# Performance work log

Hardware: AMD Instinct MI355X
Metric: run time of the kernel (lower is better)

Reference implementation:

```python
import jax, jax.numpy as jnp
import numpy as np

B, M, L = 100, 100, 8
N = M * L
EPS = 1e-5  # torch BatchNorm2d default eps


def _conv(x, w, b, stride, pad):
    y = jax.lax.conv_general_dilated(x, w, (stride, stride), [(pad, pad), (pad, pad)],
                                     dimension_numbers=('NCHW', 'OIHW', 'NCHW'))
    return y + b[None, :, None, None]


def _convT(x, w, b, stride, pad):
    # torch ConvTranspose2d weight layout: (in_ch, out_ch, kH, kW)
    k = w.shape[2]
    wt = jnp.flip(w, (2, 3)).transpose(1, 0, 2, 3)  # -> OIHW
    p = k - 1 - pad
    y = jax.lax.conv_general_dilated(x, wt, (1, 1), [(p, p), (p, p)],
                                     lhs_dilation=(stride, stride),
                                     dimension_numbers=('NCHW', 'OIHW', 'NCHW'))
    return y + b[None, :, None, None]


def _bn(x):
    # BatchNorm2d constructed fresh in forward: weight=1, bias=0, batch stats (biased var)
    mean = x.mean(axis=(0, 2, 3), keepdims=True)
    var = x.var(axis=(0, 2, 3), keepdims=True)
    return (x - mean) / jnp.sqrt(var + EPS)


def _leaky(x):
    return jnp.where(x >= 0, x, 0.01 * x)


def _forward(x, conv1_w, conv1_b, conv2_w, conv2_b, conv3_w, conv3_b, conv4_w, conv4_b,
             fc_w, fc_b, dec_w, dec_b, ct1_w, ct1_b, ct2_w, ct2_b, ct3_w, ct3_b,
             ct4_w, ct4_b, ct5_w, ct5_b):
    # ---- encoder ----
    h = _bn(_leaky(_conv(x, conv1_w, conv1_b, 2, 1)))   # (B,128,32,32)
    h = _bn(_leaky(_conv(h, conv2_w, conv2_b, 2, 1)))   # (B,256,16,16)
    h = _bn(_leaky(_conv(h, conv3_w, conv3_b, 2, 1)))   # (B,1024,8,8)
    h = _bn(_leaky(_conv(h, conv4_w, conv4_b, 2, 1)))   # (B,1024,4,4)
    eig = jax.nn.relu(h.reshape(B, -1) @ fc_w + fc_b)   # (B, 800)
    # ---- latent_sample (training branch) ----
    sig = eig.reshape(B, M, L)
    row = jnp.sqrt(float(M * L)) * jnp.fft.ifft2(sig)          # complex (B,M,L)
    # original builds C via numpy/scipy per-sample -> detached; circulant[i,j] = c[(i-j) % n]
    row_flat = jax.lax.stop_gradient(row.real.reshape(B, N))
    i = jnp.arange(N)
    idx = (i[:, None] - i[None, :]) % N                        # (N,N) circulant gather
    C = row_flat[:, idx]                                       # (B,N,N)
    # original: Sigma_batch_eps[:, i] = eigenvalue (noise zeta is dead code), via numpy -> detached
    Y = jnp.fft.fft2(jax.lax.stop_gradient(sig)).real          # (B,M,L)
    # ---- decoder ----
    d = (Y.reshape(B, N) @ dec_w + dec_b).reshape(B, 1024, 3, 3)
    d = _convT(d, ct1_w, ct1_b, 2, 1)   # (B,512,5,5)
    d = _convT(d, ct2_w, ct2_b, 2, 0)   # (B,256,11,11)
    d = _convT(d, ct3_w, ct3_b, 2, 0)   # (B,128,23,23)
    d = _convT(d, ct4_w, ct4_b, 2, 0)   # (B,64,47,47)
    d = _convT(d, ct5_w, ct5_b, 1, 0)   # (B,1,49,49)
    return d, C, eig


def setup_inputs():
    key = jax.random.key(0)
    ks = jax.random.split(key, 16)

    def wv(k, shape, fan_in):
        return (jax.random.normal(k, shape, jnp.float32) / np.sqrt(fan_in)).astype(jnp.float32)

    return {
        'x': jax.random.normal(ks[0], (B, 1, 64, 64), jnp.float32),
        'conv1_w': wv(ks[1], (128, 1, 3, 3), 9), 'conv1_b': jnp.zeros((128,), jnp.float32),
        'conv2_w': wv(ks[2], (256, 128, 3, 3), 128 * 9), 'conv2_b': jnp.zeros((256,), jnp.float32),
        'conv3_w': wv(ks[3], (1024, 256, 3, 3), 256 * 9), 'conv3_b': jnp.zeros((1024,), jnp.float32),
        'conv4_w': wv(ks[4], (1024, 1024, 3, 3), 1024 * 9), 'conv4_b': jnp.zeros((1024,), jnp.float32),
        'fc_w': wv(ks[5], (1024 * 16, N), 1024 * 16), 'fc_b': jnp.zeros((N,), jnp.float32),
        'dec_w': wv(ks[6], (N, 1024 * 9), N), 'dec_b': jnp.zeros((1024 * 9,), jnp.float32),
        'ct1_w': wv(ks[7], (1024, 512, 3, 3), 1024 * 9), 'ct1_b': jnp.zeros((512,), jnp.float32),
        'ct2_w': wv(ks[8], (512, 256, 3, 3), 512 * 9), 'ct2_b': jnp.zeros((256,), jnp.float32),
        'ct3_w': wv(ks[9], (256, 128, 3, 3), 256 * 9), 'ct3_b': jnp.zeros((128,), jnp.float32),
        'ct4_w': wv(ks[10], (128, 64, 3, 3), 128 * 9), 'ct4_b': jnp.zeros((64,), jnp.float32),
        'ct5_w': wv(ks[11], (64, 1, 3, 3), 64 * 9), 'ct5_b': jnp.zeros((1,), jnp.float32),
    }


def reference(x, conv1_w, conv1_b, conv2_w, conv2_b, conv3_w, conv3_b, conv4_w, conv4_b,
              fc_w, fc_b, dec_w, dec_b, ct1_w, ct1_b, ct2_w, ct2_b, ct3_w, ct3_b,
              ct4_w, ct4_b, ct5_w, ct5_b):
    return _forward(x, conv1_w, conv1_b, conv2_w, conv2_b, conv3_w, conv3_b, conv4_w, conv4_b,
                    fc_w, fc_b, dec_w, dec_b, ct1_w, ct1_b, ct2_w, ct2_b, ct3_w, ct3_b,
                    ct4_w, ct4_b, ct5_w, ct5_b)
```

## Files before the change

### kernel.cpp

```cpp
#include <hip/hip_runtime.h>
#include <math.h>

typedef __attribute__((ext_vector_type(8))) short bf16x8;
typedef __attribute__((ext_vector_type(4))) float f32x4;
typedef unsigned short u16;

__device__ __forceinline__ u16 f2bf(float f) {
    unsigned u = __builtin_bit_cast(unsigned, f);
    u += 0x7FFFu + ((u >> 16) & 1u);
    return (u16)(u >> 16);
}
__device__ __forceinline__ float bf2f(u16 h) {
    unsigned u = ((unsigned)h) << 16;
    return __builtin_bit_cast(float, u);
}

template<int MODE, int OUT, int BM, int BN, int SWIZ, bool STATS, bool PF>
__global__ __launch_bounds__(256, 3)
void gemm(const u16* __restrict__ Abf, const u16* __restrict__ Bw,
          const float* __restrict__ bias, void* __restrict__ outv,
          float* __restrict__ stat,
          int M, int N, int K, int lgC,
          int IH, int IW, int OH, int OW, int zchunk)
{
    constexpr int ANSEG = BM / 64, BNSEG = BN / 64;
    constexpr int RM = BM / 32, RN = BN / 32;
    __shared__ __align__(16) u16 As[4 * BM * 8];
    __shared__ __align__(16) u16 Bs[4 * BN * 8];
    const int t = threadIdx.x;
    const int lane = t & 63, wave = t >> 6;
    const int lm = lane & 15, quad = lane >> 4;
    const int wm = wave & 1, wn = wave >> 1;
    int mt, nt, z;
    if (SWIZ == 1) {
        int mtN = (M + BM - 1) / BM;
        int id = blockIdx.x;
        nt = id & 7; int j = id >> 3;
        mt = j % mtN; z = j / mtN;
    } else { mt = blockIdx.x; nt = blockIdx.y; z = blockIdx.z; }
    const int k0 = z * zchunk, kend = k0 + zchunk;

    const int arow = (ANSEG == 2) ? (t >> 1) : (t >> 2);
    const int akb  = (ANSEG == 2) ? (t & 1) * 16 : (t & 3) * 8;
    const int a_gm = mt * BM + arow;
    const bool a_in = a_gm < M;
    int oy = 0, ox = 0, bimg = 0;
    if (MODE == 1) {
        int ohw = OH * OW;
        int g = a_in ? a_gm : 0;
        bimg = g / ohw; int r = g - bimg * ohw;
        oy = r / OW; ox = r - (r / OW) * OW;
    }
    const int brow = (BNSEG == 2) ? (t >> 1) : (t >> 2);
    const int bkb  = (BNSEG == 2) ? (t & 1) * 16 : (t & 3) * 8;
    const int b_gn = nt * BN + brow;
    const bool b_in = b_gn < N;

    const int Cmask = (1 << lgC) - 1;
    int ic_s = 0, tap_s = 0;
    bool aok = a_in;
    const u16* aptr;
    if (MODE == 0) {
        aptr = Abf + (size_t)a_gm * K + k0 + akb;
    } else {
        int kk0 = k0 + akb;
        tap_s = kk0 >> lgC; ic_s = kk0 & Cmask;
        int ky = tap_s / 3, kx = tap_s - (tap_s / 3) * 3;
        int iy = oy * 2 - 1 + ky, ix = ox * 2 - 1 + kx;
        aok = a_in && (unsigned)iy < (unsigned)IH && (unsigned)ix < (unsigned)IW;
        aptr = Abf + ((((size_t)bimg * IH + iy) * IW + ix) << lgC);
    }
    const u16* bptr = Bw + (size_t)b_gn * K + k0 + bkb;

    auto ldA = [&](uint4 (&v)[ANSEG]) {
        #pragma unroll
        for (int s = 0; s < ANSEG; s++) {
            uint4 x4 = make_uint4(0, 0, 0, 0);
            if (MODE == 0) {
                if (aok) x4 = *(const uint4*)(aptr + s * 8);
            } else {
                if (aok) x4 = *(const uint4*)(aptr + ic_s + s * 8);
            }
            v[s] = x4;
        }
        if (MODE == 0) {
            aptr += 32;
        } else {
            ic_s += 32;
            if (ic_s > Cmask) {
                ic_s -= Cmask + 1;
                tap_s++;
                int ky = tap_s / 3, kx = tap_s - (tap_s / 3) * 3;
                int iy = oy * 2 - 1 + ky, ix = ox * 2 - 1 + kx;
                aok = a_in && (unsigned)iy < (unsigned)IH && (unsigned)ix < (unsigned)IW;
                aptr = Abf + ((((size_t)bimg * IH + iy) * IW + ix) << lgC);
            }
        }
    };
    auto ldB = [&](uint4 (&v)[BNSEG]) {
        #pragma unroll
        for (int s = 0; s < BNSEG; s++) {
            uint4 x4 = make_uint4(0, 0, 0, 0);
            if (b_in) x4 = *(const uint4*)(bptr + s * 8);
            v[s] = x4;
        }
        bptr += 32;
    };

    f32x4 acc[RM][RN];
    #pragma unroll
    for (int i = 0; i < RM; i++)
        #pragma unroll
        for (int j = 0; j < RN; j++) acc[i][j] = (f32x4){0.f, 0.f, 0.f, 0.f};

    uint4 va[ANSEG], vb[BNSEG];
    if (PF) { ldA(va); ldB(vb); }
    for (int kb = k0; kb < kend; kb += 32) {
        if (!PF) { ldA(va); ldB(vb); }
        #pragma unroll
        for (int s = 0; s < ANSEG; s++)
            *(uint4*)&As[(((akb >> 3) + s) * BM + arow) * 8] = va[s];
        #pragma unroll
        for (int s = 0; s < BNSEG; s++)
            *(uint4*)&Bs[(((bkb >> 3) + s) * BN + brow) * 8] = vb[s];
        __syncthreads();
        if (PF && kb + 32 < kend) { ldA(va); ldB(vb); }
        bf16x8 af[RM], bfr[RN];
        #pragma unroll
        for (int i = 0; i < RM; i++)
            af[i] = *(const bf16x8*)&As[(size_t)(quad * BM + wm * (BM / 2) + i * 16 + lm) * 8];
        #pragma unroll
        for (int j = 0; j < RN; j++)
            bfr[j] = *(const bf16x8*)&Bs[(size_t)(quad * BN + wn * (BN / 2) + j * 16 + lm) * 8];
        #pragma unroll
        for (int i = 0; i < RM; i++)
            #pragma unroll
            for (int j = 0; j < RN; j++)
                acc[i][j] = __builtin_amdgcn_mfma_f32_16x16x32_bf16(af[i], bfr[j], acc[i][j], 0, 0, 0);
        __syncthreads();
    }

    const int n_base = nt * BN + wn * (BN / 2);
    const int m_base = mt * BM + wm * (BM / 2);
    int nj[RN]; float bvj[RN];
    #pragma unroll
    for (int j = 0; j < RN; j++) {
        nj[j] = n_base + j * 16 + lm;
        bvj[j] = 0.f;
        if (nj[j] < N && OUT != 4) {
            if (OUT == 0 || OUT == 5) bvj[j] = bias[nj[j]];
            else if (z == 0) bvj[j] = bias[nj[j]];
        }
    }
    if constexpr (OUT == 4) {
        float* op = (float*)outv;
        #pragma unroll
        for (int i = 0; i < RM; i++)
            #pragma unroll
            for (int r = 0; r < 4; r++) {
                int m = m_base + i * 16 + quad * 4 + r;
                if (m >= M) continue;
                #pragma unroll
                for (int j = 0; j < RN; j++)
                    if (nj[j] < N) atomicAdd(&op[(size_t)m * N + nj[j]], acc[i][j][r]);
            }
    } else if constexpr (OUT == 5) {
        u16* op = (u16*)outv;
        #pragma unroll
        for (int j = 0; j < RN; j++) {
            if (nj[j] >= N) continue;
            int c = nj[j] / 9, hw = nj[j] - c * 9;
            #pragma unroll
            for (int i = 0; i < RM; i++)
                #pragma unroll
                for (int r = 0; r < 4; r++) {
                    int m = m_base + i * 16 + quad * 4 + r;
                    if (m >= M) continue;
                    op[((size_t)m * 9 + hw) * 1024 + c] = f2bf(acc[i][j][r] + bvj[j]);
                }
        }
    } else if constexpr (OUT == 0) {
        int ohw = OH * OW;
        float sj[RN], qj[RN];
        #pragma unroll
        for (int j = 0; j < RN; j++) { sj[j] = 0.f; qj[j] = 0.f; }
        #pragma unroll
        for (int i = 0; i < RM; i++) {
            int m0 = m_base + i * 16 + quad * 4;
            if (m0 >= M) continue;
            int b = m0 / ohw, pix = m0 - b * ohw;
            #pragma unroll
            for (int j = 0; j < RN; j++) {
                if (nj[j] >= N) continue;
                #pragma unroll
                for (int r = 0; r < 4; r++) {
                    float val = acc[i][j][r] + bvj[j];
                    ((u16*)outv)[((size_t)b * ohw + pix + r) * N + nj[j]] = f2bf(val);
                    if (STATS) {
                        float lv = val >= 0.f ? val : 0.01f * val;
                        sj[j] += lv; qj[j] += lv * lv;
                    }
                }
            }
        }
        if constexpr (STATS) {
            #pragma unroll
            for (int j = 0; j < RN; j++) {
                float s = sj[j], q = qj[j];
                s += __shfl_down(s, 32); q += __shfl_down(q, 32);
                s += __shfl_down(s, 16); q += __shfl_down(q, 16);
                if (quad == 0 && nj[j] < N) {
                    atomicAdd(&stat[nj[j]], s);
                    atomicAdd(&stat[N + nj[j]], q);
                }
            }
        }
    } else {
        int ohw = OH * OW;
        #pragma unroll
        for (int i = 0; i < RM; i++) {
            int m0 = m_base + i * 16 + quad * 4;
            if (m0 >= M) continue;
            int b = m0 / ohw, pix = m0 - b * ohw;
            #pragma unroll
            for (int j = 0; j < RN; j++) {
                if (nj[j] >= N) continue;
                #pragma unroll
                for (int r = 0; r < 4; r++)
                    atomicAdd(&((float*)outv)[((size_t)b * ohw + pix + r) * N + nj[j]],
                              acc[i][j][r] + bvj[j]);
            }
        }
    }
}

template<int BM>
__global__ __launch_bounds__(256, 3)
void gemm_ct(const u16* __restrict__ Abf, const u16* __restrict__ Wb,
             const float* __restrict__ bias, u16* __restrict__ out,
             int N, int lgC, int IH, int IW, int OH, int OW,
             int4 Kc, int4 Mc, int4 Hc, int4 Wc, int4 Oc, int4 Dy, int4 Dx)
{
    constexpr int ANSEG = BM / 64;
    constexpr int RM = BM / 32, RN = 2;
    const int c = blockIdx.z;
    const int Ks[4] = {Kc.x, Kc.y, Kc.z, Kc.w};
    const int Ms[4] = {Mc.x, Mc.y, Mc.z, Mc.w};
    const int Hs[4] = {Hc.x, Hc.y, Hc.z, Hc.w};
    const int Wsz[4]= {Wc.x, Wc.y, Wc.z, Wc.w};
    const int Os[4] = {Oc.x, Oc.y, Oc.z, Oc.w};
    const int Dys[4]= {Dy.x, Dy.y, Dy.z, Dy.w};
    const int Dxs[4]= {Dx.x, Dx.y, Dx.z, Dx.w};
    const int K = Ks[c], M = Ms[c], OHc = Hs[c], OWc = Wsz[c];
    const int dyp = Dys[c], dxp = Dxs[c];
    const int mt = blockIdx.x, nt = blockIdx.y;
    if (mt * BM >= M) return;
    const u16* Bw = Wb + Os[c];

    __shared__ __align__(16) u16 As[4 * BM * 8];
    __shared__ __align__(16) u16 Bs[4 * 64 * 8];
    const int t = threadIdx.x;
    const int lane = t & 63, wave = t >> 6;
    const int lm = lane & 15, quad = lane >> 4;
    const int wm = wave & 1, wn = wave >> 1;

    const int arow = (ANSEG == 2) ? (t >> 1) : (t >> 2);
    const int akb  = (ANSEG == 2) ? (t & 1) * 16 : (t & 3) * 8;
    const int a_gm = mt * BM + arow;
    const bool a_in = a_gm < M;
    const int ohwc = OHc * OWc;
    int g = a_in ? a_gm : 0;
    int bimg = g / ohwc; int rr = g - bimg * ohwc;
    int oy = rr / OWc, ox = rr - (rr / OWc) * OWc;

    const int brow = t >> 2;
    const int bkb  = (t & 3) * 8;
    const int b_gn = nt * 64 + brow;
    const bool b_in = b_gn < N;

    const int Cmask = (1 << lgC) - 1;
    int ic_s = akb & Cmask;
    int ti_s = 0;
    bool aok; const u16* aptr;
    {
        int sh = 8 * (ti_s & 3);
        int dy = (int)(signed char)((dyp >> sh) & 255);
        int dx = (int)(signed char)((dxp >> sh) & 255);
        int iy = oy + dy, ix = ox + dx;
        aok = a_in && (unsigned)iy < (unsigned)IH && (unsigned)ix < (unsigned)IW;
        aptr = Abf + ((((size_t)bimg * IH + iy) * IW + ix) << lgC);
    }
    const u16* bptr = Bw + (size_t)b_gn * K + bkb;

    auto ldA = [&](uint4 (&v)[ANSEG]) {
        #pragma unroll
        for (int s = 0; s < ANSEG; s++) {
            uint4 x4 = make_uint4(0, 0, 0, 0);
            if (aok) x4 = *(const uint4*)(aptr + ic_s + s * 8);
            v[s] = x4;
        }
        ic_s += 32;
        if (ic_s > Cmask) {
            ic_s -= Cmask + 1;
            ti_s++;
            int sh = 8 * (ti_s & 3);
            int dy = (int)(signed char)((dyp >> sh) & 255);
            int dx = (int)(signed char)((dxp >> sh) & 255);
            int iy = oy + dy, ix = ox + dx;
            aok = a_in && (unsigned)iy < (unsigned)IH && (unsigned)ix < (unsigned)IW;
            aptr = Abf + ((((size_t)bimg * IH + iy) * IW + ix) << lgC);
        }
    };
    auto ldB = [&](uint4& v) {
        uint4 x4 = make_uint4(0, 0, 0, 0);
        if (b_in) x4 = *(const uint4*)bptr;
        v = x4;
        bptr += 32;
    };

    f32x4 acc[RM][RN];
    #pragma unroll
    for (int i = 0; i < RM; i++)
        #pragma unroll
        for (int j = 0; j < RN; j++) acc[i][j] = (f32x4){0.f, 0.f, 0.f, 0.f};

    uint4 va[ANSEG]; uint4 vb;
    ldA(va); ldB(vb);
    for (int kb = 0; kb < K; kb += 32) {
        #pragma unroll
        for (int s = 0; s < ANSEG; s++)
            *(uint4*)&As[(((akb >> 3) + s) * BM + arow) * 8] = va[s];
        *(uint4*)&Bs[((bkb >> 3) * 64 + brow) * 8] = vb;
        __syncthreads();
        if (kb + 32 < K) { ldA(va); ldB(vb); }
        bf16x8 af[RM], bfr[RN];
        #pragma unroll
        for (int i = 0; i < RM; i++)
            af[i] = *(const bf16x8*)&As[(size_t)(quad * BM + wm * (BM / 2) + i * 16 + lm) * 8];
        #pragma unroll
        for (int j = 0; j < RN; j++)
            bfr[j] = *(const bf16x8*)&Bs[(size_t)(quad * 64 + wn * 32 + j * 16 + lm) * 8];
        #pragma unroll
        for (int i = 0; i < RM; i++)
            #pragma unroll
            for (int j = 0; j < RN; j++)
                acc[i][j] = __builtin_amdgcn_mfma_f32_16x16x32_bf16(af[i], bfr[j], acc[i][j], 0, 0, 0);
        __syncthreads();
    }

    const int n_base = nt * 64 + wn * 32;
    const int m_base = mt * BM + wm * (BM / 2);
    const int cy = c >> 1, cx = c & 1;
    const int OHW = OH * OW;
    int nj[RN]; float bvj[RN];
    #pragma unroll
    for (int j = 0; j < RN; j++) {
        nj[j] = n_base + j * 16 + lm;
        bvj[j] = (nj[j] < N) ? bias[nj[j]] : 0.f;
    }
    #pragma unroll
    for (int i = 0; i < RM; i++)
        #pragma unroll
        for (int r = 0; r < 4; r++) {
            int m = m_base + i * 16 + quad * 4 + r;
            if (m >= M) continue;
            int b = m / ohwc, r2 = m - b * ohwc;
            int oyc = r2 / OWc, oxc = r2 - (r2 / OWc) * OWc;
            size_t ad0 = ((size_t)b * OHW + (2 * oyc + cy) * OW + 2 * oxc + cx) * N;
            #pragma unroll
            for (int j = 0; j < RN; j++)
                if (nj[j] < N) out[ad0 + nj[j]] = f2bf(acc[i][j][r] + bvj[j]);
        }
}

__global__ __launch_bounds__(256)
void convw_prep(const float* __restrict__ src, u16* __restrict__ dst, int lgC, int total) {
    int idx = blockIdx.x * 256 + threadIdx.x;
    if (idx >= total) return;
    int K = 9 << lgC;
    int oc = idx / K, kk = idx - oc * K;
    int tap = kk >> lgC, ic = kk & ((1 << lgC) - 1);
    dst[idx] = f2bf(src[(((size_t)oc << lgC) + ic) * 9 + tap]);
}

__global__ __launch_bounds__(256)
void transpose_cvt(const float* __restrict__ in, u16* __restrict__ out, int R, int C) {
    __shared__ float tl[32][33];
    int c0 = blockIdx.x * 32, r0 = blockIdx.y * 32;
    int tx = threadIdx.x & 31, ty = threadIdx.x >> 5;
    #pragma unroll
    for (int l = 0; l < 4; l++)
        tl[ty + 8 * l][tx] = in[(size_t)(r0 + ty + 8 * l) * C + c0 + tx];
    __syncthreads();
    #pragma unroll
    for (int l = 0; l < 4; l++)
        out[(size_t)(c0 + ty + 8 * l) * R + r0 + tx] = f2bf(tl[tx][ty + 8 * l]);
}

__global__ __launch_bounds__(256)
void ctw_fused(const float* __restrict__ in, u16* __restrict__ outw,
               int CIN, int P, int4 Kc, int4 Oc) {
    __shared__ float tl[32][33];
    int c0 = blockIdx.x * 32, r0 = blockIdx.y * 32;
    int C = gridDim.x * 32;
    int tx = threadIdx.x & 31, ty = threadIdx.x >> 5;
    #pragma unroll
    for (int l = 0; l < 4; l++)
        tl[ty + 8 * l][tx] = in[(size_t)(r0 + ty + 8 * l) * C + c0 + tx];
    __syncthreads();
    const int Ks[4] = {Kc.x, Kc.y, Kc.z, Kc.w};
    const int Os[4] = {Oc.x, Oc.y, Oc.z, Oc.w};
    int ic = r0 + tx;
    #pragma unroll
    for (int l = 0; l < 4; l++) {
        int cc = c0 + ty + 8 * l;
        int oc = cc / 9, tap = cc - 9 * oc;
        int ky = tap / 3, kx = tap - 3 * (tap / 3);
        int cyc = (P + ky) & 1, cxc = (P + kx) & 1;
        int cls = cyc * 2 + cxc;
        int nkx = ((P ^ cxc) & 1) ? 1 : 2;
        int ti = (ky >> 1) * nkx + (kx >> 1);
        outw[Os[cls] + (size_t)oc * Ks[cls] + ti * CIN + ic] = f2bf(tl[tx][ty + 8 * l]);
    }
}

__global__ __launch_bounds__(256)
void fcw_prep(const float* __restrict__ in, u16* __restrict__ out) {
    __shared__ float tl[32][33];
    int n0 = blockIdx.x * 32, c0 = blockIdx.y * 32, hw = blockIdx.z;
    int tx = threadIdx.x & 31, ty = threadIdx.x >> 5;
    #pragma unroll
    for (int l = 0; l < 4; l++)
        tl[ty + 8 * l][tx] = in[((size_t)(c0 + ty + 8 * l) * 16 + hw) * 800 + n0 + tx];
    __syncthreads();
    #pragma unroll
    for (int l = 0; l < 4; l++)
        out[(size_t)(n0 + ty + 8 * l) * 16384 + hw * 1024 + c0 + tx] = f2bf(tl[tx][ty + 8 * l]);
}

__global__ __launch_bounds__(256)
void wt5_prep(const float* __restrict__ in, u16* __restrict__ out) {
    int idx = blockIdx.x * 256 + threadIdx.x;
    if (idx >= 576) return;
    int tap = idx >> 6, ic = idx & 63;
    out[idx] = f2bf(in[ic * 9 + tap]);
}

__global__ __launch_bounds__(256)
void conv1_nhwc(const float* __restrict__ x, const float* __restrict__ w,
                const float* __restrict__ bias, u16* __restrict__ out) {
    int idx = blockIdx.x * 256 + threadIdx.x;
    if (idx >= 100 * 1024 * 128) return;
    int oc = idx & 127;
    int pix = (idx >> 7) & 1023;
    int b = idx >> 17;
    int oy = pix >> 5, ox = pix & 31;
    int iy0 = oy * 2 - 1, ix0 = ox * 2 - 1;
    float acc = bias[oc];
    const float* ip = x + (size_t)b * 4096;
    const float* wp = w + oc * 9;
    #pragma unroll
    for (int ky = 0; ky < 3; ky++) {
        int iy = iy0 + ky;
        if ((unsigned)iy >= 64u) continue;
        #pragma unroll
        for (int kx = 0; kx < 3; kx++) {
            int ix = ix0 + kx;
            if ((unsigned)ix >= 64u) continue;
            acc = fmaf(ip[iy * 64 + ix], wp[ky * 3 + kx], acc);
        }
    }
    out[idx] = f2bf(acc);
}

__global__ __launch_bounds__(256)
void bnstat8(const u16* __restrict__ x, float* __restrict__ accum, int C, int total) {
    __shared__ float ls[2048];
    for (int i = threadIdx.x; i < 2 * C; i += 256) ls[i] = 0.f;
    __syncthreads();
    int base = (blockIdx.x * 256 + threadIdx.x) * 8;
    int stride = gridDim.x * 256 * 8;
    float s[8], q[8];
    #pragma unroll
    for (int r = 0; r < 8; r++) { s[r] = 0.f; q[r] = 0.f; }
    for (int i = base; i < total; i += stride) {
        uint4 v = *(const uint4*)(x + i);
        const unsigned* w = (const unsigned*)&v;
        #pragma unroll
        for (int h = 0; h < 4; h++) {
            float v0 = __builtin_bit_cast(float, w[h] << 16);
            float v1 = __builtin_bit_cast(float, w[h] & 0xFFFF0000u);
            v0 = v0 >= 0.f ? v0 : 0.01f * v0;
            v1 = v1 >= 0.f ? v1 : 0.01f * v1;
            s[2 * h] += v0;     q[2 * h] += v0 * v0;
            s[2 * h + 1] += v1; q[2 * h + 1] += v1 * v1;
        }
    }
    int c0 = base & (C - 1);
    #pragma unroll
    for (int r = 0; r < 8; r++) {
        atomicAdd(&ls[c0 + r], s[r]);
        atomicAdd(&ls[C + c0 + r], q[r]);
    }
    __syncthreads();
    for (int i = threadIdx.x; i < 2 * C; i += 256) atomicAdd(&accum[i], ls[i]);
}

__global__ __launch_bounds__(256)
void bnapply8(const u16* __restrict__ x, u16* __restrict__ out,
              const float* __restrict__ accum, int C, int total, float invcnt) {
    int i8 = (blockIdx.x * 256 + threadIdx.x) * 8;
    if (i8 >= total) return;
    int c0 = i8 & (C - 1);
    uint4 v = *(const uint4*)(x + i8);
    const unsigned* w = (const unsigned*)&v;
    uint4 o;
    unsigned* ow = (unsigned*)&o;
    #pragma unroll
    for (int h = 0; h < 4; h++) {
        float m0 = accum[c0 + 2 * h] * invcnt, m1 = accum[c0 + 2 * h + 1] * invcnt;
        float q0 = accum[C + c0 + 2 * h] * invcnt, q1 = accum[C + c0 + 2 * h + 1] * invcnt;
        float in0 = rsqrtf(q0 - m0 * m0 + 1e-5f);
        float in1 = rsqrtf(q1 - m1 * m1 + 1e-5f);
        float v0 = __builtin_bit_cast(float, w[h] << 16);
        float v1 = __builtin_bit_cast(float, w[h] & 0xFFFF0000u);
        v0 = v0 >= 0.f ? v0 : 0.01f * v0;
        v1 = v1 >= 0.f ? v1 : 0.01f * v1;
        unsigned r0 = f2bf((v0 - m0) * in0);
        unsigned r1 = f2bf((v1 - m1) * in1);
        ow[h] = r0 | (r1 << 16);
    }
    *(uint4*)(out + i8) = o;
}

__global__ __launch_bounds__(256)
void bnstat4f(const float* __restrict__ x, float* __restrict__ accum, int C, int total) {
    __shared__ float ls[2048];
    for (int i = threadIdx.x; i < 2 * C; i += 256) ls[i] = 0.f;
    __syncthreads();
    int base = (blockIdx.x * 256 + threadIdx.x) * 4;
    int stride = gridDim.x * 1024;
    float s[4] = {0, 0, 0, 0}, q[4] = {0, 0, 0, 0};
    for (int i = base; i < total; i += stride) {
        f32x4 v = *(const f32x4*)(x + i);
        #pragma unroll
        for (int r = 0; r < 4; r++) {
            float vv = v[r]; vv = vv >= 0.f ? vv : 0.01f * vv;
            s[r] += vv; q[r] += vv * vv;
        }
    }
    int c0 = base & (C - 1);
    #pragma unroll
    for (int r = 0; r < 4; r++) {
        atomicAdd(&ls[c0 + r], s[r]);
        atomicAdd(&ls[C + c0 + r], q[r]);
    }
    __syncthreads();
    for (int i = threadIdx.x; i < 2 * C; i += 256) atomicAdd(&accum[i], ls[i]);
}

__global__ __launch_bounds__(256)
void bnapply4f(const float* __restrict__ x, u16* __restrict__ out,
               const float* __restrict__ accum, int C, int total, float invcnt) {
    int i4 = (blockIdx.x * 256 + threadIdx.x) * 4;
    if (i4 >= total) return;
    int c0 = i4 & (C - 1);
    f32x4 v = *(const f32x4*)(x + i4);
    unsigned r4[4];
    #pragma unroll
    for (int r = 0; r < 4; r++) {
        float m = accum[c0 + r] * invcnt;
        float var = accum[C + c0 + r] * invcnt - m * m;
        float inv = rsqrtf(var + 1e-5f);
        float vv = v[r]; vv = vv >= 0.f ? vv : 0.01f * vv;
        r4[r] = f2bf((vv - m) * inv);
    }
    *(uint2*)(out + i4) = make_uint2(r4[0] | (r4[1] << 16), r4[2] | (r4[3] << 16));
}

__global__ __launch_bounds__(256)
void finalize_relu(const float* __restrict__ acc, const float* __restrict__ bias,
                   float* __restrict__ out) {
    int i = blockIdx.x * 256 + threadIdx.x;
    if (i >= 100 * 800) return;
    float v = acc[i] + bias[i % 800];
    out[i] = fmaxf(v, 0.f);
}

__global__ __launch_bounds__(256)
void dft_real(const float* __restrict__ eig, float* __restrict__ Yr, u16* __restrict__ Yrb) {
    __shared__ float se[800];
    __shared__ float ctab[800];
    int b = blockIdx.x;
    for (int i = threadIdx.x; i < 800; i += 256) {
        se[i] = eig[b * 800 + i];
        ctab[i] = cospif(i * 0.0025f);
    }
    __syncthreads();
    int o0 = blockIdx.y * 400;
    for (int oi = o0 + threadIdx.x; oi < o0 + 400; oi += 256) {
        int k1 = oi >> 3, k2 = oi & 7;
        int d1 = k1 * 8, d2 = k2 * 100;
        float acc0 = 0.f, acc1 = 0.f;
        int p1 = 0;
        for (int n1 = 0; n1 < 100; n1 += 2) {
            int p = p1;
            #pragma unroll
            for (int n2 = 0; n2 < 8; n2++) {
                acc0 = fmaf(se[n1 * 8 + n2], ctab[p], acc0);
                p += d2; if (p >= 800) p -= 800;
            }
            int pb = p1 + d1; if (pb >= 800) pb -= 800;
            int p2 = pb;
            #pragma unroll
            for (int n2 = 0; n2 < 8; n2++) {
                acc1 = fmaf(se[(n1 + 1) * 8 + n2], ctab[p2], acc1);
                p2 += d2; if (p2 >= 800) p2 -= 800;
            }
            p1 = pb + d1; if (p1 >= 800) p1 -= 800;
        }
        float acc = acc0 + acc1;
        Yr[b * 800 + oi] = acc;
        Yrb[b * 800 + oi] = f2bf(acc);
    }
}

__global__ __launch_bounds__(256)
void build_C4(const float* __restrict__ Yr, float* __restrict__ C) {
    int idx = blockIdx.x * 256 + threadIdx.x;
    if (idx >= 100 * 800 * 200) return;
    int j4 = (idx % 200) * 4; int tt = idx / 200;
    int i = tt % 800;         int b = tt / 800;
    const float* y = Yr + b * 800;
    f32x4 v;
    #pragma unroll
    for (int r = 0; r < 4; r++) {
        int k = i - (j4 + r);
        k += (k >> 31) & 800;
        v[r] = y[k] * 0.035355339059327376f;
    }
    ((f32x4*)C)[idx] = v;
}

__global__ __launch_bounds__(256)
void convT5(const u16* __restrict__ in, const u16* __restrict__ w,
            const float* __restrict__ bias, float* __restrict__ out) {
    int idx = blockIdx.x * 256 + threadIdx.x;
    if (idx >= 100 * 49 * 49) return;
    int ox = idx % 49; int t2 = idx / 49;
    int oy = t2 % 49;  int b = t2 / 49;
    float ac[8];
    #pragma unroll
    for (int r = 0; r < 8; r++) ac[r] = 0.f;
    for (int ky = 0; ky < 3; ky++) {
        int iy = oy - ky;
        if ((unsigned)iy >= 47u) continue;
        for (int kx = 0; kx < 3; kx++) {
            int ix = ox - kx;
            if ((unsigned)ix >= 47u) continue;
            const uint4* ip = (const uint4*)(in + (((size_t)b * 47 + iy) * 47 + ix) * 64);
            const uint4* wp = (const uint4*)(w + (ky * 3 + kx) * 64);
            #pragma unroll
            for (int g = 0; g < 8; g++) {
                uint4 av = ip[g], wv = wp[g];
                const unsigned* aa = (const unsigned*)&av;
                const unsigned* ww = (const unsigned*)&wv;
                #pragma unroll
                for (int h = 0; h < 4; h++) {
                    float a0 = __builtin_bit_cast(float, aa[h] << 16);
                    float a1 = __builtin_bit_cast(float, aa[h] & 0xFFFF0000u);
                    float w0 = __builtin_bit_cast(float, ww[h] << 16);
                    float w1 = __builtin_bit_cast(float, ww[h] & 0xFFFF0000u);
                    int rix = ((g & 1) << 2) | h;
                    ac[rix] = fmaf(a0, w0, ac[rix]);
                    ac[rix] = fmaf(a1, w1, ac[rix]);
                }
            }
        }
    }
    out[idx] = bias[0] + ((ac[0] + ac[1]) + (ac[2] + ac[3]))
                       + ((ac[4] + ac[5]) + (ac[6] + ac[7]));
}

struct CTClass { int T, OHc, OWc, dyp, dxp, off, K; };
static void ct_params(int P, int OH, int OW, int CIN, int OC, CTClass cls[4]) {
    int off = 0;
    for (int c = 0; c < 4; c++) {
        int cy = c >> 1, cx = c & 1;
        int kys[2], dys[2], nky = 0, kxs[2], dxs[2], nkx = 0;
        for (int ky = 0; ky < 3; ky++)
            if (((cy + P + ky) & 1) == 0) { kys[nky] = ky; dys[nky] = (cy + P - ky) / 2; nky++; }
        for (int kx = 0; kx < 3; kx++)
            if (((cx + P + kx) & 1) == 0) { kxs[nkx] = kx; dxs[nkx] = (cx + P - kx) / 2; nkx++; }
        CTClass& cc = cls[c];
        cc.T = nky * nkx;
        cc.OHc = (OH - cy + 1) >> 1; cc.OWc = (OW - cx + 1) >> 1;
        cc.dyp = 0; cc.dxp = 0;
        int ti = 0;
        for (int a = 0; a < nky; a++)
            for (int b2 = 0; b2 < nkx; b2++, ti++) {
                cc.dyp |= (dys[a] & 255) << (8 * ti);
                cc.dxp |= (dxs[b2] & 255) << (8 * ti);
            }
        cc.off = off; cc.K = CIN * cc.T;
        off += OC * cc.K;
    }
}

template<int BM>
static void launch_ct(hipStream_t s, const u16* in, const u16* W, const float* bias, u16* outp,
                      int lgC, int OC, int IH, int IW, int OH, int OW, const CTClass* cls) {
    int maxMT = 0;
    for (int c = 0; c < 4; c++) {
        int mt = (100 * cls[c].OHc * cls[c].OWc + BM - 1) / BM;
        if (mt > maxMT) maxMT = mt;
    }
    dim3 g(maxMT, (OC + 63) / 64, 4);
    gemm_ct<BM><<<g, 256, 0, s>>>(in, W, bias, outp, OC, lgC, IH, IW, OH, OW,
        make_int4(cls[0].K, cls[1].K, cls[2].K, cls[3].K),
        make_int4(100*cls[0].OHc*cls[0].OWc, 100*cls[1].OHc*cls[1].OWc,
                  100*cls[2].OHc*cls[2].OWc, 100*cls[3].OHc*cls[3].OWc),
        make_int4(cls[0].OHc, cls[1].OHc, cls[2].OHc, cls[3].OHc),
        make_int4(cls[0].OWc, cls[1].OWc, cls[2].OWc, cls[3].OWc),
        make_int4(cls[0].off, cls[1].off, cls[2].off, cls[3].off),
        make_int4(cls[0].dyp, cls[1].dyp, cls[2].dyp, cls[3].dyp),
        make_int4(cls[0].dxp, cls[1].dxp, cls[2].dxp, cls[3].dxp));
}

static void launch_ctw(hipStream_t s, const float* w, u16* outw,
                       int CIN, int OC, int P, const CTClass* cls) {
    dim3 g((OC * 9) / 32, CIN / 32);
    ctw_fused<<<g, 256, 0, s>>>(w, outw, CIN, P,
        make_int4(cls[0].K, cls[1].K, cls[2].K, cls[3].K),
        make_int4(cls[0].off, cls[1].off, cls[2].off, cls[3].off));
}

extern "C" void kernel_launch(void* const* d_in, const int* in_sizes, int n_in,
                              void* d_out, int out_size, void* d_ws, size_t ws_size,
                              hipStream_t stream) {
    const float* x    = (const float*)d_in[0];
    const float* c1w  = (const float*)d_in[1];  const float* c1b = (const float*)d_in[2];
    const float* c2w  = (const float*)d_in[3];  const float* c2b = (const float*)d_in[4];
    const float* c3w  = (const float*)d_in[5];  const float* c3b = (const float*)d_in[6];
    const float* c4w  = (const float*)d_in[7];  const float* c4b = (const float*)d_in[8];
    const float* fcw  = (const float*)d_in[9];  const float* fcb = (const float*)d_in[10];
    const float* decw = (const float*)d_in[11]; const float* decb = (const float*)d_in[12];
    const float* t1w  = (const float*)d_in[13]; const float* t1b = (const float*)d_in[14];
    const float* t2w  = (const float*)d_in[15]; const float* t2b = (const float*)d_in[16];
    const float* t3w  = (const float*)d_in[17]; const float* t3b = (const float*)d_in[18];
    const float* t4w  = (const float*)d_in[19]; const float* t4b = (const float*)d_in[20];
    const float* t5w  = (const float*)d_in[21]; const float* t5b = (const float*)d_in[22];

    float* out = (float*)d_out;
    float* d_final = out;
    float* Cmat    = out + 240100;
    float* eig     = out + 240100 + 64000000;

    float* ws = (float*)d_ws;
    u16*   h1    = (u16*)(ws);
    u16*   W_fc  = (u16*)(ws);
    u16*   h2    = (u16*)(ws + 6553600);
    u16*   h3    = (u16*)(ws + 9830400);
    u16*   W_c2  = (u16*)(ws + 13107200);
    u16*   W_c3  = (u16*)(ws + 13254656);
    u16*   W_c4  = (u16*)(ws + 14434304);
    float* h4f   = ws + 19152896;
    u16*   h4    = (u16*)(ws + 20791296);
    float* accs  = ws + 21610496;
    float* facc  = ws + 21618688;
    float* Yr    = ws + 21698688;
    u16*   Yrb   = (u16*)(ws + 21778688);
    u16*   d0    = (u16*)(ws + 21818688);
    u16*   W_dec = (u16*)(ws + 22279488);
    float* acc1 = accs, *acc2 = accs + 2048, *acc3 = accs + 4096, *acc4 = accs + 6144;
    u16*   W_t   = (u16*)(ws);
    u16*   o1    = (u16*)(ws + 4718592);
    u16*   o2    = (u16*)(ws + 5358592);
    u16*   o3    = (u16*)(ws + 6907392);
    u16*   o4    = (u16*)(ws + 10292992);
    u16*   W_t5  = (u16*)(ws + 17361792);

    #define GRID(n) dim3(((n) + 255) / 256)

    hipMemsetAsync(accs, 0, (8192 + 80000) * 4, stream);

    conv1_nhwc<<<GRID(13107200), 256, 0, stream>>>(x, c1w, c1b, h1);
    bnstat8<<<1024, 256, 0, stream>>>(h1, acc1, 128, 13107200);
    bnapply8<<<GRID(1638400), 256, 0, stream>>>(h1, h1, acc1, 128, 13107200, 1.f / 102400.f);

    convw_prep<<<GRID(294912), 256, 0, stream>>>(c2w, W_c2, 7, 294912);
    gemm<1, 0, 128, 128, 0, true, false><<<dim3(200, 2, 1), 256, 0, stream>>>(
        h1, W_c2, c2b, h2, acc2, 25600, 256, 1152, 7, 32, 32, 16, 16, 1152);
    bnapply8<<<GRID(819200), 256, 0, stream>>>(h2, h2, acc2, 256, 6553600, 1.f / 25600.f);

    convw_prep<<<GRID(2359296), 256, 0, stream>>>(c3w, W_c3, 8, 2359296);
    gemm<1, 0, 128, 128, 1, true, false><<<dim3(400, 1, 1), 256, 0, stream>>>(
        h2, W_c3, c3b, h3, acc3, 6400, 1024, 2304, 8, 16, 16, 8, 8, 2304);
    bnapply8<<<GRID(819200), 256, 0, stream>>>(h3, h3, acc3, 1024, 6553600, 1.f / 6400.f);

    convw_prep<<<GRID(9437184), 256, 0, stream>>>(c4w, W_c4, 10, 9437184);
    hipMemsetAsync(h4f, 0, 1638400 * 4, stream);
    gemm<1, 1, 64, 128, 1, false, true><<<dim3(400, 1, 1), 256, 0, stream>>>(
        h3, W_c4, c4b, h4f, nullptr, 1600, 1024, 9216, 10, 8, 8, 4, 4, 4608);
    bnstat4f<<<1024, 256, 0, stream>>>(h4f, acc4, 1024, 1638400);
    bnapply4f<<<GRID(409600), 256, 0, stream>>>(h4f, h4, acc4, 1024, 1638400, 1.f / 1600.f);

    fcw_prep<<<dim3(25, 32, 16), 256, 0, stream>>>(fcw, W_fc);
    gemm<0, 4, 64, 64, 0, false, true><<<dim3(2, 13, 16), 256, 0, stream>>>(
        h4, W_fc, nullptr, facc, nullptr, 100, 800, 16384, 0, 0, 0, 0, 0, 1024);
    finalize_relu<<<GRID(80000), 256, 0, stream>>>(facc, fcb, eig);

    dft_real<<<dim3(100, 2), 256, 0, stream>>>(eig, Yr, Yrb);
    build_C4<<<GRID(16000000), 256, 0, stream>>>(Yr, Cmat);

    transpose_cvt<<<dim3(288, 25), 256, 0, stream>>>(decw, W_dec, 800, 9216);
    gemm<0, 5, 64, 64, 0, false, true><<<dim3(2, 144, 1), 256, 0, stream>>>(
        Yrb, W_dec, decb, d0, nullptr, 100, 9216, 800, 0, 0, 0, 0, 0, 800);

    CTClass c1c[4], c2c[4], c3c[4], c4c[4];
    ct_params(1, 5, 5, 1024, 512, c1c);
    ct_params(0, 11, 11, 512, 256, c2c);
    ct_params(0, 23, 23, 256, 128, c3c);
    ct_params(0, 47, 47, 128, 64, c4c);

    launch_ctw(stream, t1w, W_t, 1024, 512, 1, c1c);
    launch_ct<64>(stream, d0, W_t, t1b, o1, 10, 512, 3, 3, 5, 5, c1c);

    launch_ctw(stream, t2w, W_t, 512, 256, 0, c2c);
    launch_ct<64>(stream, o1, W_t, t2b, o2, 9, 256, 5, 5, 11, 11, c2c);

    launch_ctw(stream, t3w, W_t, 256, 128, 0, c3c);
    launch_ct<64>(stream, o2, W_t, t3b, o3, 8, 128, 11, 11, 23, 23, c3c);

    launch_ctw(stream, t4w, W_t, 128, 64, 0, c4c);
    launch_ct<128>(stream, o3, W_t, t4b, o4, 7, 64, 23, 23, 47, 47, c4c);

    wt5_prep<<<GRID(576), 256, 0, stream>>>(t5w, W_t5);
    convT5<<<GRID(240100), 256, 0, stream>>>(o4, W_t5, t5b, d_final);

    #undef GRID
}
```

Measured before the change: 1.134 ms.

## Load GEMM tiles via global_load_lds, retile transposed convs, smem-staged weight prep

```diff
diff --git a/kernel.cpp b/kernel.cpp
--- a/kernel.cpp
+++ b/kernel.cpp
@@ -13,6 +13,14 @@
 __device__ __forceinline__ float bf2f(u16 h) {
     unsigned u = ((unsigned)h) << 16;
     return __builtin_bit_cast(float, u);
+}
+
+__device__ __align__(64) unsigned g_zeros[16];
+
+__device__ __forceinline__ void gll16(const u16* g, u16* l) {
+    __builtin_amdgcn_global_load_lds(
+        (const __attribute__((address_space(1))) unsigned*)g,
+        (__attribute__((address_space(3))) unsigned*)l, 16, 0, 0);
 }
 
 template<int MODE, int OUT, int BM, int BN, int SWIZ, bool STATS, bool PF>
@@ -23,10 +31,12 @@
           int M, int N, int K, int lgC,
           int IH, int IW, int OH, int OW, int zchunk)
 {
-    constexpr int ANSEG = BM / 64, BNSEG = BN / 64;
+    constexpr int ANSEG = BM / 64;
+    constexpr int ACALLS = BM / 64;
+    constexpr int BCALLS = BN / 64;
     constexpr int RM = BM / 32, RN = BN / 32;
-    __shared__ __align__(16) u16 As[4 * BM * 8];
-    __shared__ __align__(16) u16 Bs[4 * BN * 8];
+    __shared__ __align__(16) u16 As[BM * 32];
+    __shared__ __align__(16) u16 Bs[BN * 32];
     const int t = threadIdx.x;
     const int lane = t & 63, wave = t >> 6;
     const int lm = lane & 15, quad = lane >> 4;
@@ -40,29 +50,44 @@
     } else { mt = blockIdx.x; nt = blockIdx.y; z = blockIdx.z; }
     const int k0 = z * zchunk, kend = k0 + zchunk;
 
+    const int sl_row  = (wave << 4) + (lane >> 2);
+    const int sl_koff = (lane & 3) * 8;
+
+    const u16* bsrc[BCALLS]; int bmask[BCALLS];
+    #pragma unroll
+    for (int s = 0; s < BCALLS; s++) {
+        int rg = nt * BN + s * 64 + sl_row;
+        bool ok = rg < N;
+        bsrc[s] = ok ? (Bw + (size_t)rg * K + sl_koff)
+                     : ((const u16*)g_zeros + sl_koff);
+        bmask[s] = ok ? ~0 : 0;
+    }
+
+    const u16* asrc[ACALLS]; int amask[ACALLS];
+    if constexpr (MODE == 0) {
+        #pragma unroll
+        for (int s = 0; s < ACALLS; s++) {
+            int rg = mt * BM + s * 64 + sl_row;
+            bool ok = rg < M;
+            asrc[s] = ok ? (Abf + (size_t)rg * K + sl_koff)
+                         : ((const u16*)g_zeros + sl_koff);
+            amask[s] = ok ? ~0 : 0;
+        }
+    }
     const int arow = (ANSEG == 2) ? (t >> 1) : (t >> 2);
     const int akb  = (ANSEG == 2) ? (t & 1) * 16 : (t & 3) * 8;
     const int a_gm = mt * BM + arow;
     const bool a_in = a_gm < M;
     int oy = 0, ox = 0, bimg = 0;
-    if (MODE == 1) {
+    const int Cmask = (1 << lgC) - 1;
+    int ic_s = 0, tap_s = 0;
+    bool aok = a_in;
+    const u16* aptr = Abf;
+    if constexpr (MODE == 1) {
         int ohw = OH * OW;
         int g = a_in ? a_gm : 0;
         bimg = g / ohw; int r = g - bimg * ohw;
         oy = r / OW; ox = r - (r / OW) * OW;
-    }
-    const int brow = (BNSEG == 2) ? (t >> 1) : (t >> 2);
-    const int bkb  = (BNSEG == 2) ? (t & 1) * 16 : (t & 3) * 8;
-    const int b_gn = nt * BN + brow;
-    const bool b_in = b_gn < N;
-
-    const int Cmask = (1 << lgC) - 1;
-    int ic_s = 0, tap_s = 0;
-    bool aok = a_in;
-    const u16* aptr;
-    if (MODE == 0) {
-        aptr = Abf + (size_t)a_gm * K + k0 + akb;
-    } else {
         int kk0 = k0 + akb;
         tap_s = kk0 >> lgC; ic_s = kk0 & Cmask;
         int ky = tap_s / 3, kx = tap_s - (tap_s / 3) * 3;
@@ -70,68 +95,61 @@
         aok = a_in && (unsigned)iy < (unsigned)IH && (unsigned)ix < (unsigned)IW;
         aptr = Abf + ((((size_t)bimg * IH + iy) * IW + ix) << lgC);
     }
-    const u16* bptr = Bw + (size_t)b_gn * K + k0 + bkb;
-
     auto ldA = [&](uint4 (&v)[ANSEG]) {
         #pragma unroll
         for (int s = 0; s < ANSEG; s++) {
             uint4 x4 = make_uint4(0, 0, 0, 0);
-            if (MODE == 0) {
-                if (aok) x4 = *(const uint4*)(aptr + s * 8);
-            } else {
-                if (aok) x4 = *(const uint4*)(aptr + ic_s + s * 8);
-            }
+            if (aok) x4 = *(const uint4*)(aptr + ic_s + s * 8);
             v[s] = x4;
         }
-        if (MODE == 0) {
-            aptr += 32;
+        ic_s += 32;
+        if (ic_s > Cmask) {
+            ic_s -= Cmask + 1;
+            tap_s++;
+            int ky = tap_s / 3, kx = tap_s - (tap_s / 3) * 3;
+            int iy = oy * 2 - 1 + ky, ix = ox * 2 - 1 + kx;
+            aok = a_in && (unsigned)iy < (unsigned)IH && (unsigned)ix < (unsigned)IW;
+            aptr = Abf + ((((size_t)bimg * IH + iy) * IW + ix) << lgC);
+        }
+    };
+
+    f32x4 acc[RM][RN];
+    #pragma unroll
+    for (int i = 0; i < RM; i++)
+        #pragma unroll
+        for (int j = 0; j < RN; j++) acc[i][j] = (f32x4){0.f, 0.f, 0.f, 0.f};
+
+    uint4 va[ANSEG];
+    if (MODE == 1 && PF) ldA(va);
+    for (int kb = k0; kb < kend; kb += 32) {
+        if constexpr (MODE == 1) {
+            if (!PF) ldA(va);
+            #pragma unroll
+            for (int s = 0; s < ANSEG; s++)
+                *(uint4*)&As[(((akb >> 3) + s) * BM + arow) * 8] = va[s];
         } else {
-            ic_s += 32;
-            if (ic_s > Cmask) {
-                ic_s -= Cmask + 1;
-                tap_s++;
-                int ky = tap_s / 3, kx = tap_s - (tap_s / 3) * 3;
-                int iy = oy * 2 - 1 + ky, ix = ox * 2 - 1 + kx;
-                aok = a_in && (unsigned)iy < (unsigned)IH && (unsigned)ix < (unsigned)IW;
-                aptr = Abf + ((((size_t)bimg * IH + iy) * IW + ix) << lgC);
-            }
-        }
-    };
-    auto ldB = [&](uint4 (&v)[BNSEG]) {
-        #pragma unroll
-        for (int s = 0; s < BNSEG; s++) {
-            uint4 x4 = make_uint4(0, 0, 0, 0);
-            if (b_in) x4 = *(const uint4*)(bptr + s * 8);
-            v[s] = x4;
-        }
-        bptr += 32;
-    };
-
-    f32x4 acc[RM][RN];
-    #pragma unroll
-    for (int i = 0; i < RM; i++)
-        #pragma unroll
-        for (int j = 0; j < RN; j++) acc[i][j] = (f32x4){0.f, 0.f, 0.f, 0.f};
-
-    uint4 va[ANSEG], vb[BNSEG];
-    if (PF) { ldA(va); ldB(vb); }
-    for (int kb = k0; kb < kend; kb += 32) {
-        if (!PF) { ldA(va); ldB(vb); }
-        #pragma unroll
-        for (int s = 0; s < ANSEG; s++)
-            *(uint4*)&As[(((akb >> 3) + s) * BM + arow) * 8] = va[s];
-        #pragma unroll
-        for (int s = 0; s < BNSEG; s++)
-            *(uint4*)&Bs[(((bkb >> 3) + s) * BN + brow) * 8] = vb[s];
+            #pragma unroll
+            for (int s = 0; s < ACALLS; s++)
+                gll16(asrc[s] + (kb & amask[s]),
+                      &As[(size_t)(s * 64 + (wave << 4)) * 32]);
+        }
+        #pragma unroll
+        for (int s = 0; s < BCALLS; s++)
+            gll16(bsrc[s] + (kb & bmask[s]),
+                  &Bs[(size_t)(s * 64 + (wave << 4)) * 32]);
         __syncthreads();
-        if (PF && kb + 32 < kend) { ldA(va); ldB(vb); }
+        if (MODE == 1 && PF && kb + 32 < kend) ldA(va);
         bf16x8 af[RM], bfr[RN];
         #pragma unroll
-        for (int i = 0; i < RM; i++)
-            af[i] = *(const bf16x8*)&As[(size_t)(quad * BM + wm * (BM / 2) + i * 16 + lm) * 8];
+        for (int i = 0; i < RM; i++) {
+            if constexpr (MODE == 0)
+                af[i] = *(const bf16x8*)&As[(wm * (BM / 2) + i * 16 + lm) * 32 + quad * 8];
+            else
+                af[i] = *(const bf16x8*)&As[(size_t)(quad * BM + wm * (BM / 2) + i * 16 + lm) * 8];
+        }
         #pragma unroll
         for (int j = 0; j < RN; j++)
-            bfr[j] = *(const bf16x8*)&Bs[(size_t)(quad * BN + wn * (BN / 2) + j * 16 + lm) * 8];
+            bfr[j] = *(const bf16x8*)&Bs[(wn * (BN / 2) + j * 16 + lm) * 32 + quad * 8];
         #pragma unroll
         for (int i = 0; i < RM; i++)
             #pragma unroll
@@ -234,7 +252,7 @@
     }
 }
 
-template<int BM>
+template<int BM, int BN>
 __global__ __launch_bounds__(256, 3)
 void gemm_ct(const u16* __restrict__ Abf, const u16* __restrict__ Wb,
              const float* __restrict__ bias, u16* __restrict__ out,
@@ -242,7 +260,8 @@
              int4 Kc, int4 Mc, int4 Hc, int4 Wc, int4 Oc, int4 Dy, int4 Dx)
 {
     constexpr int ANSEG = BM / 64;
-    constexpr int RM = BM / 32, RN = 2;
+    constexpr int BCALLS = BN / 64;
+    constexpr int RM = BM / 32, RN = BN / 32;
     const int c = blockIdx.z;
     const int Ks[4] = {Kc.x, Kc.y, Kc.z, Kc.w};
     const int Ms[4] = {Mc.x, Mc.y, Mc.z, Mc.w};
@@ -257,12 +276,21 @@
     if (mt * BM >= M) return;
     const u16* Bw = Wb + Os[c];
 
-    __shared__ __align__(16) u16 As[4 * BM * 8];
-    __shared__ __align__(16) u16 Bs[4 * 64 * 8];
+    __shared__ __align__(16) u16 As[BM * 32];
+    __shared__ __align__(16) u16 Bs[BN * 32];
     const int t = threadIdx.x;
     const int lane = t & 63, wave = t >> 6;
     const int lm = lane & 15, quad = lane >> 4;
     const int wm = wave & 1, wn = wave >> 1;
+
+    const int sl_row  = (wave << 4) + (lane >> 2);
+    const int sl_koff = (lane & 3) * 8;
+    const u16* bsrc[BCALLS];
+    #pragma unroll
+    for (int s = 0; s < BCALLS; s++) {
+        int rg = nt * BN + s * 64 + sl_row;
+        bsrc[s] = Bw + (size_t)rg * K + sl_koff;
+    }
 
     const int arow = (ANSEG == 2) ? (t >> 1) : (t >> 2);
     const int akb  = (ANSEG == 2) ? (t & 1) * 16 : (t & 3) * 8;
@@ -272,11 +300,6 @@
     int g = a_in ? a_gm : 0;
     int bimg = g / ohwc; int rr = g - bimg * ohwc;
     int oy = rr / OWc, ox = rr - (rr / OWc) * OWc;
-
-    const int brow = t >> 2;
-    const int bkb  = (t & 3) * 8;
-    const int b_gn = nt * 64 + brow;
-    const bool b_in = b_gn < N;
 
     const int Cmask = (1 << lgC) - 1;
     int ic_s = akb & Cmask;
@@ -290,8 +313,6 @@
         aok = a_in && (unsigned)iy < (unsigned)IH && (unsigned)ix < (unsigned)IW;
         aptr = Abf + ((((size_t)bimg * IH + iy) * IW + ix) << lgC);
     }
-    const u16* bptr = Bw + (size_t)b_gn * K + bkb;
-
     auto ldA = [&](uint4 (&v)[ANSEG]) {
         #pragma unroll
         for (int s = 0; s < ANSEG; s++) {
@@ -311,12 +332,6 @@
             aptr = Abf + ((((size_t)bimg * IH + iy) * IW + ix) << lgC);
         }
     };
-    auto ldB = [&](uint4& v) {
-        uint4 x4 = make_uint4(0, 0, 0, 0);
-        if (b_in) x4 = *(const uint4*)bptr;
-        v = x4;
-        bptr += 32;
-    };
 
     f32x4 acc[RM][RN];
     #pragma unroll
@@ -324,22 +339,24 @@
         #pragma unroll
         for (int j = 0; j < RN; j++) acc[i][j] = (f32x4){0.f, 0.f, 0.f, 0.f};
 
-    uint4 va[ANSEG]; uint4 vb;
-    ldA(va); ldB(vb);
+    uint4 va[ANSEG];
+    ldA(va);
     for (int kb = 0; kb < K; kb += 32) {
         #pragma unroll
         for (int s = 0; s < ANSEG; s++)
             *(uint4*)&As[(((akb >> 3) + s) * BM + arow) * 8] = va[s];
-        *(uint4*)&Bs[((bkb >> 3) * 64 + brow) * 8] = vb;
+        #pragma unroll
+        for (int s = 0; s < BCALLS; s++)
+            gll16(bsrc[s] + kb, &Bs[(size_t)(s * 64 + (wave << 4)) * 32]);
         __syncthreads();
-        if (kb + 32 < K) { ldA(va); ldB(vb); }
+        if (kb + 32 < K) ldA(va);
         bf16x8 af[RM], bfr[RN];
         #pragma unroll
         for (int i = 0; i < RM; i++)
             af[i] = *(const bf16x8*)&As[(size_t)(quad * BM + wm * (BM / 2) + i * 16 + lm) * 8];
         #pragma unroll
         for (int j = 0; j < RN; j++)
-            bfr[j] = *(const bf16x8*)&Bs[(size_t)(quad * 64 + wn * 32 + j * 16 + lm) * 8];
+            bfr[j] = *(const bf16x8*)&Bs[(wn * (BN / 2) + j * 16 + lm) * 32 + quad * 8];
         #pragma unroll
         for (int i = 0; i < RM; i++)
             #pragma unroll
@@ -348,7 +365,7 @@
         __syncthreads();
     }
 
-    const int n_base = nt * 64 + wn * 32;
+    const int n_base = nt * BN + wn * (BN / 2);
     const int m_base = mt * BM + wm * (BM / 2);
     const int cy = c >> 1, cx = c & 1;
     const int OHW = OH * OW;
@@ -374,13 +391,17 @@
 }
 
 __global__ __launch_bounds__(256)
-void convw_prep(const float* __restrict__ src, u16* __restrict__ dst, int lgC, int total) {
-    int idx = blockIdx.x * 256 + threadIdx.x;
-    if (idx >= total) return;
-    int K = 9 << lgC;
-    int oc = idx / K, kk = idx - oc * K;
-    int tap = kk >> lgC, ic = kk & ((1 << lgC) - 1);
-    dst[idx] = f2bf(src[(((size_t)oc << lgC) + ic) * 9 + tap]);
+void convw_prep(const float* __restrict__ src, u16* __restrict__ dst, int lgC) {
+    __shared__ float tl[9216];
+    int CIN = 1 << lgC;
+    int n = CIN * 9;
+    size_t base = (size_t)blockIdx.x * n;
+    for (int i = threadIdx.x; i < n; i += 256) tl[i] = src[base + i];
+    __syncthreads();
+    for (int j = threadIdx.x; j < n; j += 256) {
+        int tap = j >> lgC, ic = j & (CIN - 1);
+        dst[base + j] = f2bf(tl[ic * 9 + tap]);
+    }
 }
 
 __global__ __launch_bounds__(256)
@@ -707,7 +728,7 @@
     }
 }
 
-template<int BM>
+template<int BM, int BN>
 static void launch_ct(hipStream_t s, const u16* in, const u16* W, const float* bias, u16* outp,
                       int lgC, int OC, int IH, int IW, int OH, int OW, const CTClass* cls) {
     int maxMT = 0;
@@ -715,8 +736,8 @@
         int mt = (100 * cls[c].OHc * cls[c].OWc + BM - 1) / BM;
         if (mt > maxMT) maxMT = mt;
     }
-    dim3 g(maxMT, (OC + 63) / 64, 4);
-    gemm_ct<BM><<<g, 256, 0, s>>>(in, W, bias, outp, OC, lgC, IH, IW, OH, OW,
+    dim3 g(maxMT, OC / BN, 4);
+    gemm_ct<BM, BN><<<g, 256, 0, s>>>(in, W, bias, outp, OC, lgC, IH, IW, OH, OW,
         make_int4(cls[0].K, cls[1].K, cls[2].K, cls[3].K),
         make_int4(100*cls[0].OHc*cls[0].OWc, 100*cls[1].OHc*cls[1].OWc,
                   100*cls[2].OHc*cls[2].OWc, 100*cls[3].OHc*cls[3].OWc),
@@ -788,17 +809,17 @@
     bnstat8<<<1024, 256, 0, stream>>>(h1, acc1, 128, 13107200);
     bnapply8<<<GRID(1638400), 256, 0, stream>>>(h1, h1, acc1, 128, 13107200, 1.f / 102400.f);
 
-    convw_prep<<<GRID(294912), 256, 0, stream>>>(c2w, W_c2, 7, 294912);
+    convw_prep<<<dim3(256), 256, 0, stream>>>(c2w, W_c2, 7);
     gemm<1, 0, 128, 128, 0, true, false><<<dim3(200, 2, 1), 256, 0, stream>>>(
         h1, W_c2, c2b, h2, acc2, 25600, 256, 1152, 7, 32, 32, 16, 16, 1152);
     bnapply8<<<GRID(819200), 256, 0, stream>>>(h2, h2, acc2, 256, 6553600, 1.f / 25600.f);
 
-    convw_prep<<<GRID(2359296), 256, 0, stream>>>(c3w, W_c3, 8, 2359296);
+    convw_prep<<<dim3(1024), 256, 0, stream>>>(c3w, W_c3, 8);
     gemm<1, 0, 128, 128, 1, true, false><<<dim3(400, 1, 1), 256, 0, stream>>>(
         h2, W_c3, c3b, h3, acc3, 6400, 1024, 2304, 8, 16, 16, 8, 8, 2304);
     bnapply8<<<GRID(819200), 256, 0, stream>>>(h3, h3, acc3, 1024, 6553600, 1.f / 6400.f);
 
-    convw_prep<<<GRID(9437184), 256, 0, stream>>>(c4w, W_c4, 10, 9437184);
+    convw_prep<<<dim3(1024), 256, 0, stream>>>(c4w, W_c4, 10);
     hipMemsetAsync(h4f, 0, 1638400 * 4, stream);
     gemm<1, 1, 64, 128, 1, false, true><<<dim3(400, 1, 1), 256, 0, stream>>>(
         h3, W_c4, c4b, h4f, nullptr, 1600, 1024, 9216, 10, 8, 8, 4, 4, 4608);
@@ -806,7 +827,7 @@
     bnapply4f<<<GRID(409600), 256, 0, stream>>>(h4f, h4, acc4, 1024, 1638400, 1.f / 1600.f);
 
     fcw_prep<<<dim3(25, 32, 16), 256, 0, stream>>>(fcw, W_fc);
-    gemm<0, 4, 64, 64, 0, false, true><<<dim3(2, 13, 16), 256, 0, stream>>>(
+    gemm<0, 4, 64, 64, 0, false, false><<<dim3(2, 13, 16), 256, 0, stream>>>(
         h4, W_fc, nullptr, facc, nullptr, 100, 800, 16384, 0, 0, 0, 0, 0, 1024);
     finalize_relu<<<GRID(80000), 256, 0, stream>>>(facc, fcb, eig);
 
@@ -814,7 +835,7 @@
     build_C4<<<GRID(16000000), 256, 0, stream>>>(Yr, Cmat);
 
     transpose_cvt<<<dim3(288, 25), 256, 0, stream>>>(decw, W_dec, 800, 9216);
-    gemm<0, 5, 64, 64, 0, false, true><<<dim3(2, 144, 1), 256, 0, stream>>>(
+    gemm<0, 5, 64, 64, 0, false, false><<<dim3(2, 144, 1), 256, 0, stream>>>(
         Yrb, W_dec, decb, d0, nullptr, 100, 9216, 800, 0, 0, 0, 0, 0, 800);
 
     CTClass c1c[4], c2c[4], c3c[4], c4c[4];
@@ -824,16 +845,16 @@
     ct_params(0, 47, 47, 128, 64, c4c);
 
     launch_ctw(stream, t1w, W_t, 1024, 512, 1, c1c);
-    launch_ct<64>(stream, d0, W_t, t1b, o1, 10, 512, 3, 3, 5, 5, c1c);
+    launch_ct<64, 64>(stream, d0, W_t, t1b, o1, 10, 512, 3, 3, 5, 5, c1c);
 
     launch_ctw(stream, t2w, W_t, 512, 256, 0, c2c);
-    launch_ct<64>(stream, o1, W_t, t2b, o2, 9, 256, 5, 5, 11, 11, c2c);
+    launch_ct<64, 128>(stream, o1, W_t, t2b, o2, 9, 256, 5, 5, 11, 11, c2c);
 
     launch_ctw(stream, t3w, W_t, 256, 128, 0, c3c);
-    launch_ct<64>(stream, o2, W_t, t3b, o3, 8, 128, 11, 11, 23, 23, c3c);
+    launch_ct<64, 128>(stream, o2, W_t, t3b, o3, 8, 128, 11, 11, 23, 23, c3c);
 
     launch_ctw(stream, t4w, W_t, 128, 64, 0, c4c);
-    launch_ct<128>(stream, o3, W_t, t4b, o4, 7, 64, 23, 23, 47, 47, c4c);
+    launch_ct<128, 64>(stream, o3, W_t, t4b, o4, 7, 64, 23, 23, 47, 47, c4c);
 
     wt5_prep<<<GRID(576), 256, 0, stream>>>(t5w, W_t5);
     convT5<<<GRID(240100), 256, 0, stream>>>(o4, W_t5, t5b, d_final);
```

New measurement: 1.134 ms. Within noise of the previous version (-0.0%).
